# Performance work log

Hardware: AMD Instinct MI355X
Metric: run time of the kernel (lower is better)

The kernel has to match this reference:

```python
import jax, jax.numpy as jnp
import numpy as np

EPS = 1e-5


def conv1x1(x, w, b):
    # x: [b,c,h,w], w: [o,c], b: [o] -> [b,o,h,w]  (1x1 conv == channel matmul)
    return jnp.einsum('bchw,oc->bohw', x, w) + b[None, :, None, None]


def nor_mean_std(x):
    # instance norm over spatial dims (torch calc_mean_std uses unbiased var)
    mean = jnp.mean(x, axis=(2, 3), keepdims=True)
    var = jnp.var(x, axis=(2, 3), keepdims=True, ddof=1)
    return (x - mean) / jnp.sqrt(var + EPS)


def nor_mean(x):
    mean = jnp.mean(x, axis=(2, 3), keepdims=True)
    return x - mean, mean


def net(x, w1, b1, w2, b2):
    return conv1x1(jax.nn.relu(conv1x1(x, w1, b1)), w2, b2)


def setup_inputs() -> dict:
    key = jax.random.key(0)
    ks = jax.random.split(key, 8)
    B, C, H, W = 8, 256, 128, 128
    return {
        'content': jax.random.normal(ks[0], (B, C, H, W), jnp.float32),
        'style': jax.random.normal(ks[1], (B, C, H, W), jnp.float32),
        'w1': jax.random.normal(ks[2], (128, 256), jnp.float32) * 0.05,
        'b1': jax.random.normal(ks[3], (128,), jnp.float32) * 0.05,
        'w2': jax.random.normal(ks[4], (32, 128), jnp.float32) * 0.05,
        'b2': jax.random.normal(ks[5], (32,), jnp.float32) * 0.05,
        'wu': jax.random.normal(ks[6], (256, 32), jnp.float32) * 0.05,
        'bu': jax.random.normal(ks[7], (256,), jnp.float32) * 0.05,
    }


def reference(content, style, w1, b1, w2, b2, wu, bu):
    cF_nor = nor_mean_std(content)
    sF_nor, smean = nor_mean(style)
    cF = net(cF_nor, w1, b1, w2, b2)          # [b,32,h,w]
    sF = net(sF_nor, w1, b1, w2, b2)          # [b,32,h,w]
    b, c, h, w = cF.shape
    hw = h * w
    sf = sF.reshape(b, c, hw)
    # channel covariance: [b,32,32]
    s_cov = jnp.einsum('bcn,bdn->bcd', sf, sf) / hw
    s_cov = jax.nn.softmax(s_cov, axis=-1) * (c ** -0.5)
    gF = jnp.einsum('bcd,bdn->bcn', s_cov, cF.reshape(b, c, hw)).reshape(b, c, h, w)
    gF = conv1x1(gF, wu, bu)                  # [b,256,h,w]
    return gF + smean + content
```

## Files before the change

### kernel.cpp

```cpp
#include <hip/hip_runtime.h>

#define HW 16384
#define C_IN 256
#define C_MID 128
#define C_OUT 32
#define EPSF 1e-5f

typedef __bf16 bf16x8 __attribute__((ext_vector_type(8)));
typedef __bf16 bf16x4 __attribute__((ext_vector_type(4)));
typedef float f32x4 __attribute__((ext_vector_type(4)));

__device__ __forceinline__ bf16x4 cvt4(f32x4 v) {
    bf16x4 r;
    r[0] = (__bf16)v[0]; r[1] = (__bf16)v[1];
    r[2] = (__bf16)v[2]; r[3] = (__bf16)v[3];
    return r;
}

__global__ __launch_bounds__(512) void k_stats10(const float* __restrict__ content,
                                                 const float* __restrict__ style,
                                                 float* __restrict__ cmean,
                                                 float* __restrict__ crstd,
                                                 float* __restrict__ smean,
                                                 __bf16* __restrict__ cbf,
                                                 __bf16* __restrict__ sbf) {
    const int bc = blockIdx.x;
    const int t = threadIdx.x;
    const f32x4* cp = (const f32x4*)(content + (size_t)bc * HW);
    const f32x4* sp = (const f32x4*)(style + (size_t)bc * HW);
    const int phase = (bc * 257) & 4095;

    int idx[8];
    #pragma unroll
    for (int i = 0; i < 8; ++i) idx[i] = (phase + t + i * 512) & 4095;

    f32x4 c[8], s[8];
    #pragma unroll
    for (int i = 0; i < 8; ++i) c[i] = __builtin_nontemporal_load(cp + idx[i]);
    #pragma unroll
    for (int i = 0; i < 8; ++i) s[i] = __builtin_nontemporal_load(sp + idx[i]);
    asm volatile("" ::
        "v"(c[0]), "v"(c[1]), "v"(c[2]), "v"(c[3]), "v"(c[4]), "v"(c[5]), "v"(c[6]), "v"(c[7]),
        "v"(s[0]), "v"(s[1]), "v"(s[2]), "v"(s[3]), "v"(s[4]), "v"(s[5]), "v"(s[6]), "v"(s[7]));

    {
        bf16x4* cb = (bf16x4*)(cbf + (size_t)bc * HW);
        bf16x4* sb = (bf16x4*)(sbf + (size_t)bc * HW);
        #pragma unroll
        for (int i = 0; i < 8; ++i) {
            cb[idx[i]] = cvt4(c[i]);
            sb[idx[i]] = cvt4(s[i]);
        }
    }

    float cs, cq, ss;
    {
        f32x4 a01 = c[0] + c[1], a23 = c[2] + c[3], a45 = c[4] + c[5], a67 = c[6] + c[7];
        f32x4 a = (a01 + a23) + (a45 + a67);
        cs = (a[0] + a[1]) + (a[2] + a[3]);
        f32x4 q01 = c[0]*c[0] + c[1]*c[1], q23 = c[2]*c[2] + c[3]*c[3];
        f32x4 q45 = c[4]*c[4] + c[5]*c[5], q67 = c[6]*c[6] + c[7]*c[7];
        f32x4 q = (q01 + q23) + (q45 + q67);
        cq = (q[0] + q[1]) + (q[2] + q[3]);
        f32x4 b01 = s[0] + s[1], b23 = s[2] + s[3], b45 = s[4] + s[5], b67 = s[6] + s[7];
        f32x4 bsum = (b01 + b23) + (b45 + b67);
        ss = (bsum[0] + bsum[1]) + (bsum[2] + bsum[3]);
    }

    #pragma unroll
    for (int d = 32; d > 0; d >>= 1) {
        cs += __shfl_xor(cs, d, 64);
        cq += __shfl_xor(cq, d, 64);
        ss += __shfl_xor(ss, d, 64);
    }
    __shared__ float rs[8], rq[8], rss[8];
    const int wv = t >> 6;
    if ((t & 63) == 0) { rs[wv] = cs; rq[wv] = cq; rss[wv] = ss; }
    __syncthreads();
    if (t == 0) {
        float S = 0.f, Q = 0.f, SS = 0.f;
        #pragma unroll
        for (int i = 0; i < 8; ++i) { S += rs[i]; Q += rq[i]; SS += rss[i]; }
        float n = (float)HW;
        float var = (Q - S * S / n) / (n - 1.f);
        cmean[bc] = S / n;
        crstd[bc] = 1.f / sqrtf(var + EPSF);
        smean[bc] = SS / n;
    }
}

__global__ __launch_bounds__(256) void k_wprep2(const float* __restrict__ w1,
                                                const float* __restrict__ b1,
                                                const float* __restrict__ w2,
                                                const float* __restrict__ cmean,
                                                const float* __restrict__ crstd,
                                                const float* __restrict__ smean,
                                                __bf16* __restrict__ W1c,
                                                float* __restrict__ bias1c,
                                                __bf16* __restrict__ W1s,
                                                float* __restrict__ bias1s,
                                                __bf16* __restrict__ W2b) {
    int o = blockIdx.x, b = blockIdx.y, t = threadIdx.x;
    float w = w1[o * 256 + t];
    float r = crstd[b * 256 + t];
    float wc = w * r;
    W1c[((size_t)(b * 128 + o)) * 256 + t] = (__bf16)wc;
    if (b == 0) {
        W1s[o * 256 + t] = (__bf16)w;
        if (t < 32) W2b[o * 32 + t] = (__bf16)w2[o * 32 + t];
    }
    float pc = wc * cmean[b * 256 + t];
    float ps = w * smean[b * 256 + t];
    __shared__ float rA[256], rB[256];
    rA[t] = pc; rB[t] = ps;
    __syncthreads();
    for (int off = 128; off > 0; off >>= 1) {
        if (t < off) { rA[t] += rA[t + off]; rB[t] += rB[t + off]; }
        __syncthreads();
    }
    if (t == 0) {
        bias1c[b * 128 + o] = b1[o] - rA[0];
        bias1s[b * 128 + o] = b1[o] - rB[0];
    }
}

__global__ __launch_bounds__(256) void k_net_s(const __bf16* __restrict__ x,
                                               const __bf16* __restrict__ W1,
                                               const float* __restrict__ bias1,
                                               const __bf16* __restrict__ W2,
                                               const float* __restrict__ b2,
                                               float* __restrict__ partial) {
    __shared__ __bf16 Xl[64 * 256];
    __shared__ __bf16 Tl[64 * 128];
    const int tid = threadIdx.x;
    const int l = tid & 63, wv = tid >> 6;
    const int lr = l & 15, g = l >> 4;
    const int sw = (lr & 7) << 4;
    const int p0 = blockIdx.x * 64;
    const int b = blockIdx.y;
    const __bf16* xb = x + (size_t)b * C_IN * HW;

    {
        const int p = wv * 16 + lr;
        const __bf16* xp = xb + p0 + p;
        char* row = (char*)&Xl[p * 256];
        #pragma unroll 4
        for (int cc = 0; cc < 16; ++cc) {
            const int c = cc * 16 + g * 4;
            bf16x4 v;
            v[0] = xp[(size_t)(c + 0) * HW];
            v[1] = xp[(size_t)(c + 1) * HW];
            v[2] = xp[(size_t)(c + 2) * HW];
            v[3] = xp[(size_t)(c + 3) * HW];
            *(bf16x4*)(row + ((c * 2) ^ sw)) = v;
        }
    }
    __syncthreads();

    const f32x4 zero4 = {0.f, 0.f, 0.f, 0.f};
    f32x4 acc[2][4];
    #pragma unroll
    for (int mt = 0; mt < 2; ++mt)
        #pragma unroll
        for (int nt = 0; nt < 4; ++nt) acc[mt][nt] = zero4;

    const __bf16* wrow0 = W1 + (size_t)(wv * 32 + lr) * 256 + g * 8;
    const __bf16* wrow1 = wrow0 + 16 * 256;

    #pragma unroll
    for (int kt = 0; kt < 8; ++kt) {
        bf16x8 a0 = *(const bf16x8*)(wrow0 + kt * 32);
        bf16x8 a1 = *(const bf16x8*)(wrow1 + kt * 32);
        #pragma unroll
        for (int nt = 0; nt < 4; ++nt) {
            const char* xrow = (const char*)&Xl[(nt * 16 + lr) * 256];
            bf16x8 bfr = *(const bf16x8*)(xrow + (((kt * 32 + g * 8) * 2) ^ sw));
            acc[0][nt] = __builtin_amdgcn_mfma_f32_16x16x32_bf16(a0, bfr, acc[0][nt], 0, 0, 0);
            acc[1][nt] = __builtin_amdgcn_mfma_f32_16x16x32_bf16(a1, bfr, acc[1][nt], 0, 0, 0);
        }
    }

    float4 bia[2];
    bia[0] = *(const float4*)&bias1[b * 128 + wv * 32 + g * 4];
    bia[1] = *(const float4*)&bias1[b * 128 + wv * 32 + 16 + g * 4];
    __syncthreads();
    #pragma unroll
    for (int mt = 0; mt < 2; ++mt) {
        #pragma unroll
        for (int nt = 0; nt < 4; ++nt) {
            const int p = nt * 16 + lr;
            char* trow = (char*)&Tl[p * 128];
            const int ob = (wv * 32 + mt * 16 + g * 4) * 2;
            bf16x4 tv;
            tv[0] = (__bf16)fmaxf(acc[mt][nt][0] + bia[mt].x, 0.f);
            tv[1] = (__bf16)fmaxf(acc[mt][nt][1] + bia[mt].y, 0.f);
            tv[2] = (__bf16)fmaxf(acc[mt][nt][2] + bia[mt].z, 0.f);
            tv[3] = (__bf16)fmaxf(acc[mt][nt][3] + bia[mt].w, 0.f);
            *(bf16x4*)(trow + (ob ^ sw)) = tv;
        }
    }
    __syncthreads();

    f32x4 acc2[2];
    acc2[0] = zero4; acc2[1] = zero4;
    const int p = wv * 16 + lr;
    const char* trow = (const char*)&Tl[p * 128];
    const __bf16* w2r0 = W2 + (size_t)lr * 128 + g * 8;
    const __bf16* w2r1 = w2r0 + 16 * 128;
    #pragma unroll
    for (int kt = 0; kt < 4; ++kt) {
        bf16x8 bfr = *(const bf16x8*)(trow + (((kt * 32 + g * 8) * 2) ^ sw));
        bf16x8 a0 = *(const bf16x8*)(w2r0 + kt * 32);
        bf16x8 a1 = *(const bf16x8*)(w2r1 + kt * 32);
        acc2[0] = __builtin_amdgcn_mfma_f32_16x16x32_bf16(a0, bfr, acc2[0], 0, 0, 0);
        acc2[1] = __builtin_amdgcn_mfma_f32_16x16x32_bf16(a1, bfr, acc2[1], 0, 0, 0);
    }
    float4 bb0 = *(const float4*)&b2[g * 4];
    float4 bb1 = *(const float4*)&b2[16 + g * 4];
    const int o0 = g * 4;

    float* gt = (float*)Xl;
    gt[(o0 + 0) * 65 + p] = acc2[0][0] + bb0.x;
    gt[(o0 + 1) * 65 + p] = acc2[0][1] + bb0.y;
    gt[(o0 + 2) * 65 + p] = acc2[0][2] + bb0.z;
    gt[(o0 + 3) * 65 + p] = acc2[0][3] + bb0.w;
    gt[(16 + o0 + 0) * 65 + p] = acc2[1][0] + bb1.x;
    gt[(16 + o0 + 1) * 65 + p] = acc2[1][1] + bb1.y;
    gt[(16 + o0 + 2) * 65 + p] = acc2[1][2] + bb1.z;
    gt[(16 + o0 + 3) * 65 + p] = acc2[1][3] + bb1.w;
    __syncthreads();
    const int gi = tid >> 3, jb = (tid & 7) * 4;
    float g4[4] = {0.f, 0.f, 0.f, 0.f};
    #pragma unroll 8
    for (int n = 0; n < 64; ++n) {
        float si = gt[gi * 65 + n];
        #pragma unroll
        for (int q = 0; q < 4; ++q)
            g4[q] = fmaf(si, gt[(jb + q) * 65 + n], g4[q]);
    }
    float* dst = partial + ((size_t)(b * 256 + blockIdx.x)) * 1024 + tid * 4;
    #pragma unroll
    for (int q = 0; q < 4; ++q) dst[q] = g4[q];
}

__global__ __launch_bounds__(1024) void k_softmax2(const float* __restrict__ partial,
                                                   float* __restrict__ scov) {
    int b = blockIdx.x;
    int j = threadIdx.x, i = threadIdx.y;
    const float* base = partial + (size_t)b * 256 * 1024 + i * 32 + j;
    float v0 = 0.f, v1 = 0.f, v2 = 0.f, v3 = 0.f;
    #pragma unroll 4
    for (int s = 0; s < 256; s += 4) {
        v0 += base[(s + 0) * 1024];
        v1 += base[(s + 1) * 1024];
        v2 += base[(s + 2) * 1024];
        v3 += base[(s + 3) * 1024];
    }
    float v = ((v0 + v1) + (v2 + v3)) * (1.f / (float)HW);
    float m = v;
    #pragma unroll
    for (int d = 16; d > 0; d >>= 1) m = fmaxf(m, __shfl_xor(m, d, 32));
    float e = expf(v - m);
    float sum = e;
    #pragma unroll
    for (int d = 16; d > 0; d >>= 1) sum += __shfl_xor(sum, d, 32);
    scov[(size_t)b * 1024 + i * 32 + j] = e / sum * 0.17677669529663687f;
}

__global__ __launch_bounds__(256) void k_netc_final(const __bf16* __restrict__ x,
                                                    const __bf16* __restrict__ W1,
                                                    const float* __restrict__ bias1,
                                                    const __bf16* __restrict__ W2,
                                                    const float* __restrict__ b2,
                                                    const float* __restrict__ scov,
                                                    const float* __restrict__ wu,
                                                    const float* __restrict__ bu,
                                                    const float* __restrict__ smean,
                                                    float* __restrict__ out) {
    __shared__ __bf16 Xl[64 * 256];
    __shared__ __bf16 Tl[64 * 128];
    __shared__ float sCov[1024];
    __shared__ float sG[32 * 64];
    const int tid = threadIdx.x;
    const int l = tid & 63, wv = tid >> 6;
    const int lr = l & 15, g = l >> 4;
    const int sw = (lr & 7) << 4;
    const int p0 = blockIdx.x * 64;
    const int b = blockIdx.y;
    const __bf16* xb = x + (size_t)b * C_IN * HW;

    #pragma unroll
    for (int q = 0; q < 4; ++q)
        sCov[tid + 256 * q] = scov[(size_t)b * 1024 + tid + 256 * q];
    {
        const int p = wv * 16 + lr;
        const __bf16* xp = xb + p0 + p;
        char* row = (char*)&Xl[p * 256];
        #pragma unroll 4
        for (int cc = 0; cc < 16; ++cc) {
            const int c = cc * 16 + g * 4;
            bf16x4 v;
            v[0] = xp[(size_t)(c + 0) * HW];
            v[1] = xp[(size_t)(c + 1) * HW];
            v[2] = xp[(size_t)(c + 2) * HW];
            v[3] = xp[(size_t)(c + 3) * HW];
            *(bf16x4*)(row + ((c * 2) ^ sw)) = v;
        }
    }
    __syncthreads();

    const f32x4 zero4 = {0.f, 0.f, 0.f, 0.f};
    f32x4 acc1[2][4];
    #pragma unroll
    for (int mt = 0; mt < 2; ++mt)
        #pragma unroll
        for (int nt = 0; nt < 4; ++nt) acc1[mt][nt] = zero4;

    const __bf16* W1b = W1 + ((size_t)b << 15);
    const __bf16* wrow0 = W1b + (size_t)(wv * 32 + lr) * 256 + g * 8;
    const __bf16* wrow1 = wrow0 + 16 * 256;

    #pragma unroll
    for (int kt = 0; kt < 8; ++kt) {
        bf16x8 a0 = *(const bf16x8*)(wrow0 + kt * 32);
        bf16x8 a1 = *(const bf16x8*)(wrow1 + kt * 32);
        #pragma unroll
        for (int nt = 0; nt < 4; ++nt) {
            const char* xrow = (const char*)&Xl[(nt * 16 + lr) * 256];
            bf16x8 bfr = *(const bf16x8*)(xrow + (((kt * 32 + g * 8) * 2) ^ sw));
            acc1[0][nt] = __builtin_amdgcn_mfma_f32_16x16x32_bf16(a0, bfr, acc1[0][nt], 0, 0, 0);
            acc1[1][nt] = __builtin_amdgcn_mfma_f32_16x16x32_bf16(a1, bfr, acc1[1][nt], 0, 0, 0);
        }
    }

    float4 bia[2];
    bia[0] = *(const float4*)&bias1[b * 128 + wv * 32 + g * 4];
    bia[1] = *(const float4*)&bias1[b * 128 + wv * 32 + 16 + g * 4];
    #pragma unroll
    for (int mt = 0; mt < 2; ++mt) {
        #pragma unroll
        for (int nt = 0; nt < 4; ++nt) {
            const int p = nt * 16 + lr;
            char* trow = (char*)&Tl[p * 128];
            const int ob = (wv * 32 + mt * 16 + g * 4) * 2;
            bf16x4 tv;
            tv[0] = (__bf16)fmaxf(acc1[mt][nt][0] + bia[mt].x, 0.f);
            tv[1] = (__bf16)fmaxf(acc1[mt][nt][1] + bia[mt].y, 0.f);
            tv[2] = (__bf16)fmaxf(acc1[mt][nt][2] + bia[mt].z, 0.f);
            tv[3] = (__bf16)fmaxf(acc1[mt][nt][3] + bia[mt].w, 0.f);
            *(bf16x4*)(trow + (ob ^ sw)) = tv;
        }
    }
    __syncthreads();

    f32x4 acc2[2];
    acc2[0] = zero4; acc2[1] = zero4;
    const int p = wv * 16 + lr;
    {
        const char* trow = (const char*)&Tl[p * 128];
        const __bf16* w2r0 = W2 + (size_t)lr * 128 + g * 8;
        const __bf16* w2r1 = w2r0 + 16 * 128;
        #pragma unroll
        for (int kt = 0; kt < 4; ++kt) {
            bf16x8 bfr = *(const bf16x8*)(trow + (((kt * 32 + g * 8) * 2) ^ sw));
            bf16x8 a0 = *(const bf16x8*)(w2r0 + kt * 32);
            bf16x8 a1 = *(const bf16x8*)(w2r1 + kt * 32);
            acc2[0] = __builtin_amdgcn_mfma_f32_16x16x32_bf16(a0, bfr, acc2[0], 0, 0, 0);
            acc2[1] = __builtin_amdgcn_mfma_f32_16x16x32_bf16(a1, bfr, acc2[1], 0, 0, 0);
        }
    }
    float4 bb0 = *(const float4*)&b2[g * 4];
    float4 bb1 = *(const float4*)&b2[16 + g * 4];
    const int o0 = g * 4;

    __syncthreads();
    float* sC = (float*)Tl;
    sC[(o0 + 0) * 64 + p] = acc2[0][0] + bb0.x;
    sC[(o0 + 1) * 64 + p] = acc2[0][1] + bb0.y;
    sC[(o0 + 2) * 64 + p] = acc2[0][2] + bb0.z;
    sC[(o0 + 3) * 64 + p] = acc2[0][3] + bb0.w;
    sC[(16 + o0 + 0) * 64 + p] = acc2[1][0] + bb1.x;
    sC[(16 + o0 + 1) * 64 + p] = acc2[1][1] + bb1.y;
    sC[(16 + o0 + 2) * 64 + p] = acc2[1][2] + bb1.z;
    sC[(16 + o0 + 3) * 64 + p] = acc2[1][3] + bb1.w;
    __syncthreads();

    {
        int gp = tid & 63, gib = (tid >> 6) * 8;
        #pragma unroll
        for (int rr = 0; rr < 8; ++rr) {
            int gi = gib + rr;
            float a = 0.f;
            #pragma unroll
            for (int k = 0; k < 32; ++k)
                a = fmaf(sCov[gi * 32 + k], sC[k * 64 + gp], a);
            sG[gi * 64 + gp] = a;
        }
    }
    __syncthreads();

    const int tx = tid & 7, ty = tid >> 3;
    const float* wurow = wu + (size_t)(ty * 8) * 32;
    float acc[8][8];
    #pragma unroll
    for (int i = 0; i < 8; ++i)
        #pragma unroll
        for (int j = 0; j < 8; ++j) acc[i][j] = 0.f;
    #pragma unroll 4
    for (int k = 0; k < 32; ++k) {
        float a[8];
        #pragma unroll
        for (int i = 0; i < 8; ++i) a[i] = wurow[i * 32 + k];
        float4 b4a = *(const float4*)&sG[k * 64 + tx * 8];
        float4 b4b = *(const float4*)&sG[k * 64 + tx * 8 + 4];
        float bb[8] = {b4a.x, b4a.y, b4a.z, b4a.w, b4b.x, b4b.y, b4b.z, b4b.w};
        #pragma unroll
        for (int i = 0; i < 8; ++i)
            #pragma unroll
            for (int j = 0; j < 8; ++j)
                acc[i][j] = fmaf(a[i], bb[j], acc[i][j]);
    }
    float cvv[8][8];
    #pragma unroll
    for (int j = 0; j < 8; ++j) {
        const int pl = tx * 8 + j;
        bf16x8 rv = *(const bf16x8*)((const char*)Xl + pl * 512 + ((ty * 16) ^ (j << 4)));
        #pragma unroll
        for (int i = 0; i < 8; ++i) cvv[i][j] = (float)rv[i];
    }
    #pragma unroll
    for (int i = 0; i < 8; ++i) {
        int o = ty * 8 + i;
        float add = bu[o] + smean[b * 256 + o];
        float* dst = out + (size_t)b * C_IN * HW + (size_t)o * HW + p0 + tx * 8;
        f32x4 r0 = {acc[i][0] + add + cvv[i][0], acc[i][1] + add + cvv[i][1],
                    acc[i][2] + add + cvv[i][2], acc[i][3] + add + cvv[i][3]};
        f32x4 r1 = {acc[i][4] + add + cvv[i][4], acc[i][5] + add + cvv[i][5],
                    acc[i][6] + add + cvv[i][6], acc[i][7] + add + cvv[i][7]};
        __builtin_nontemporal_store(r0, (f32x4*)dst);
        __builtin_nontemporal_store(r1, (f32x4*)(dst + 4));
    }
}

extern "C" void kernel_launch(void* const* d_in, const int* in_sizes, int n_in,
                              void* d_out, int out_size, void* d_ws, size_t ws_size,
                              hipStream_t stream) {
    const float* content = (const float*)d_in[0];
    const float* style   = (const float*)d_in[1];
    const float* w1      = (const float*)d_in[2];
    const float* b1      = (const float*)d_in[3];
    const float* w2      = (const float*)d_in[4];
    const float* b2      = (const float*)d_in[5];
    const float* wu      = (const float*)d_in[6];
    const float* bu      = (const float*)d_in[7];
    float* out = (float*)d_out;
    float* ws  = (float*)d_ws;

    float* cmean   = ws;
    float* crstd   = ws + 2048;
    float* smean   = ws + 4096;
    float* scov    = ws + 6144;
    float* bias1c  = ws + 14336;
    float* bias1s  = ws + 15360;
    __bf16* W2b    = (__bf16*)(ws + 16384);
    __bf16* W1s    = (__bf16*)(ws + 18432);
    __bf16* W1c    = (__bf16*)(ws + 34816);
    float* partial = ws + 165888;
    __bf16* cbf    = (__bf16*)(ws + 2263040);
    __bf16* sbf    = (__bf16*)(ws + 19040256);

    k_stats10<<<dim3(2048), 512, 0, stream>>>(content, style, cmean, crstd, smean, cbf, sbf);
    k_wprep2<<<dim3(128, 8), 256, 0, stream>>>(w1, b1, w2, cmean, crstd, smean,
                                               W1c, bias1c, W1s, bias1s, W2b);
    k_net_s<<<dim3(256, 8), 256, 0, stream>>>(sbf, W1s, bias1s, W2b, b2, partial);
    k_softmax2<<<dim3(8), dim3(32, 32), 0, stream>>>(partial, scov);
    k_netc_final<<<dim3(256, 8), 256, 0, stream>>>(cbf, W1c, bias1c, W2b, b2,
                                                   scov, wu, bu, smean, out);
}
```

Baseline: 223.0 us.

## Split stats and weight-prep into style and content passes reordered for cache reuse

Splits the combined statistics kernel and the weight-prep kernel into separate style and content versions. The content versions are scheduled after the style network and softmax, right before the final content kernel. The aim is for content data and its bf16 copy to still be resident in last-level cache when the final kernel reads them. It adds two extra kernel launches and smaller per-kernel memory parallelism.

Result: no change. 224.2 us (+0.6%).

```diff
diff --git a/kernel.cpp b/kernel.cpp
--- a/kernel.cpp
+++ b/kernel.cpp
@@ -17,16 +17,11 @@
     return r;
 }
 
-__global__ __launch_bounds__(512) void k_stats10(const float* __restrict__ content,
-                                                 const float* __restrict__ style,
-                                                 float* __restrict__ cmean,
-                                                 float* __restrict__ crstd,
+__global__ __launch_bounds__(512) void k_stats_s(const float* __restrict__ style,
                                                  float* __restrict__ smean,
-                                                 __bf16* __restrict__ cbf,
                                                  __bf16* __restrict__ sbf) {
     const int bc = blockIdx.x;
     const int t = threadIdx.x;
-    const f32x4* cp = (const f32x4*)(content + (size_t)bc * HW);
     const f32x4* sp = (const f32x4*)(style + (size_t)bc * HW);
     const int phase = (bc * 257) & 4095;
 
@@ -34,94 +29,135 @@
     #pragma unroll
     for (int i = 0; i < 8; ++i) idx[i] = (phase + t + i * 512) & 4095;
 
-    f32x4 c[8], s[8];
-    #pragma unroll
-    for (int i = 0; i < 8; ++i) c[i] = __builtin_nontemporal_load(cp + idx[i]);
+    f32x4 s[8];
     #pragma unroll
     for (int i = 0; i < 8; ++i) s[i] = __builtin_nontemporal_load(sp + idx[i]);
     asm volatile("" ::
-        "v"(c[0]), "v"(c[1]), "v"(c[2]), "v"(c[3]), "v"(c[4]), "v"(c[5]), "v"(c[6]), "v"(c[7]),
-        "v"(s[0]), "v"(s[1]), "v"(s[2]), "v"(s[3]), "v"(s[4]), "v"(s[5]), "v"(s[6]), "v"(s[7]));
+        "v"(s[0]), "v"(s[1]), "v"(s[2]), "v"(s[3]),
+        "v"(s[4]), "v"(s[5]), "v"(s[6]), "v"(s[7]));
+
+    {
+        bf16x4* sb = (bf16x4*)(sbf + (size_t)bc * HW);
+        #pragma unroll
+        for (int i = 0; i < 8; ++i) sb[idx[i]] = cvt4(s[i]);
+    }
+
+    f32x4 a01 = s[0] + s[1], a23 = s[2] + s[3], a45 = s[4] + s[5], a67 = s[6] + s[7];
+    f32x4 a = (a01 + a23) + (a45 + a67);
+    float ss = (a[0] + a[1]) + (a[2] + a[3]);
+
+    #pragma unroll
+    for (int d = 32; d > 0; d >>= 1) ss += __shfl_xor(ss, d, 64);
+    __shared__ float rss[8];
+    const int wv = t >> 6;
+    if ((t & 63) == 0) rss[wv] = ss;
+    __syncthreads();
+    if (t == 0) {
+        float S = 0.f;
+        #pragma unroll
+        for (int i = 0; i < 8; ++i) S += rss[i];
+        smean[bc] = S / (float)HW;
+    }
+}
+
+__global__ __launch_bounds__(512) void k_stats_c(const float* __restrict__ content,
+                                                 float* __restrict__ cmean,
+                                                 float* __restrict__ crstd,
+                                                 __bf16* __restrict__ cbf) {
+    const int bc = blockIdx.x;
+    const int t = threadIdx.x;
+    const f32x4* cp = (const f32x4*)(content + (size_t)bc * HW);
+    const int phase = (bc * 257) & 4095;
+
+    int idx[8];
+    #pragma unroll
+    for (int i = 0; i < 8; ++i) idx[i] = (phase + t + i * 512) & 4095;
+
+    f32x4 c[8];
+    #pragma unroll
+    for (int i = 0; i < 8; ++i) c[i] = __builtin_nontemporal_load(cp + idx[i]);
+    asm volatile("" ::
+        "v"(c[0]), "v"(c[1]), "v"(c[2]), "v"(c[3]),
+        "v"(c[4]), "v"(c[5]), "v"(c[6]), "v"(c[7]));
 
     {
         bf16x4* cb = (bf16x4*)(cbf + (size_t)bc * HW);
-        bf16x4* sb = (bf16x4*)(sbf + (size_t)bc * HW);
-        #pragma unroll
-        for (int i = 0; i < 8; ++i) {
-            cb[idx[i]] = cvt4(c[i]);
-            sb[idx[i]] = cvt4(s[i]);
-        }
-    }
-
-    float cs, cq, ss;
-    {
-        f32x4 a01 = c[0] + c[1], a23 = c[2] + c[3], a45 = c[4] + c[5], a67 = c[6] + c[7];
-        f32x4 a = (a01 + a23) + (a45 + a67);
-        cs = (a[0] + a[1]) + (a[2] + a[3]);
-        f32x4 q01 = c[0]*c[0] + c[1]*c[1], q23 = c[2]*c[2] + c[3]*c[3];
-        f32x4 q45 = c[4]*c[4] + c[5]*c[5], q67 = c[6]*c[6] + c[7]*c[7];
-        f32x4 q = (q01 + q23) + (q45 + q67);
-        cq = (q[0] + q[1]) + (q[2] + q[3]);
-        f32x4 b01 = s[0] + s[1], b23 = s[2] + s[3], b45 = s[4] + s[5], b67 = s[6] + s[7];
-        f32x4 bsum = (b01 + b23) + (b45 + b67);
-        ss = (bsum[0] + bsum[1]) + (bsum[2] + bsum[3]);
-    }
+        #pragma unroll
+        for (int i = 0; i < 8; ++i) cb[idx[i]] = cvt4(c[i]);
+    }
+
+    f32x4 a01 = c[0] + c[1], a23 = c[2] + c[3], a45 = c[4] + c[5], a67 = c[6] + c[7];
+    f32x4 a = (a01 + a23) + (a45 + a67);
+    float cs = (a[0] + a[1]) + (a[2] + a[3]);
+    f32x4 q01 = c[0]*c[0] + c[1]*c[1], q23 = c[2]*c[2] + c[3]*c[3];
+    f32x4 q45 = c[4]*c[4] + c[5]*c[5], q67 = c[6]*c[6] + c[7]*c[7];
+    f32x4 q = (q01 + q23) + (q45 + q67);
+    float cq = (q[0] + q[1]) + (q[2] + q[3]);
 
     #pragma unroll
     for (int d = 32; d > 0; d >>= 1) {
         cs += __shfl_xor(cs, d, 64);
         cq += __shfl_xor(cq, d, 64);
-        ss += __shfl_xor(ss, d, 64);
-    }
-    __shared__ float rs[8], rq[8], rss[8];
+    }
+    __shared__ float rs[8], rq[8];
     const int wv = t >> 6;
-    if ((t & 63) == 0) { rs[wv] = cs; rq[wv] = cq; rss[wv] = ss; }
+    if ((t & 63) == 0) { rs[wv] = cs; rq[wv] = cq; }
     __syncthreads();
     if (t == 0) {
-        float S = 0.f, Q = 0.f, SS = 0.f;
-        #pragma unroll
-        for (int i = 0; i < 8; ++i) { S += rs[i]; Q += rq[i]; SS += rss[i]; }
+        float S = 0.f, Q = 0.f;
+        #pragma unroll
+        for (int i = 0; i < 8; ++i) { S += rs[i]; Q += rq[i]; }
         float n = (float)HW;
         float var = (Q - S * S / n) / (n - 1.f);
         cmean[bc] = S / n;
         crstd[bc] = 1.f / sqrtf(var + EPSF);
-        smean[bc] = SS / n;
-    }
-}
-
-__global__ __launch_bounds__(256) void k_wprep2(const float* __restrict__ w1,
-                                                const float* __restrict__ b1,
-                                                const float* __restrict__ w2,
-                                                const float* __restrict__ cmean,
-                                                const float* __restrict__ crstd,
-                                                const float* __restrict__ smean,
-                                                __bf16* __restrict__ W1c,
-                                                float* __restrict__ bias1c,
-                                                __bf16* __restrict__ W1s,
-                                                float* __restrict__ bias1s,
-                                                __bf16* __restrict__ W2b) {
+    }
+}
+
+__global__ __launch_bounds__(256) void k_wprep_s(const float* __restrict__ w1,
+                                                 const float* __restrict__ b1,
+                                                 const float* __restrict__ w2,
+                                                 const float* __restrict__ smean,
+                                                 __bf16* __restrict__ W1s,
+                                                 float* __restrict__ bias1s,
+                                                 __bf16* __restrict__ W2b) {
+    int o = blockIdx.x, b = blockIdx.y, t = threadIdx.x;
+    float w = w1[o * 256 + t];
+    if (b == 0) {
+        W1s[o * 256 + t] = (__bf16)w;
+        if (t < 32) W2b[o * 32 + t] = (__bf16)w2[o * 32 + t];
+    }
+    float ps = w * smean[b * 256 + t];
+    __shared__ float rB[256];
+    rB[t] = ps;
+    __syncthreads();
+    for (int off = 128; off > 0; off >>= 1) {
+        if (t < off) rB[t] += rB[t + off];
+        __syncthreads();
+    }
+    if (t == 0) bias1s[b * 128 + o] = b1[o] - rB[0];
+}
+
+__global__ __launch_bounds__(256) void k_wprep_c(const float* __restrict__ w1,
+                                                 const float* __restrict__ b1,
+                                                 const float* __restrict__ cmean,
+                                                 const float* __restrict__ crstd,
+                                                 __bf16* __restrict__ W1c,
+                                                 float* __restrict__ bias1c) {
     int o = blockIdx.x, b = blockIdx.y, t = threadIdx.x;
     float w = w1[o * 256 + t];
     float r = crstd[b * 256 + t];
     float wc = w * r;
     W1c[((size_t)(b * 128 + o)) * 256 + t] = (__bf16)wc;
-    if (b == 0) {
-        W1s[o * 256 + t] = (__bf16)w;
-        if (t < 32) W2b[o * 32 + t] = (__bf16)w2[o * 32 + t];
-    }
     float pc = wc * cmean[b * 256 + t];
-    float ps = w * smean[b * 256 + t];
-    __shared__ float rA[256], rB[256];
-    rA[t] = pc; rB[t] = ps;
+    __shared__ float rA[256];
+    rA[t] = pc;
     __syncthreads();
     for (int off = 128; off > 0; off >>= 1) {
-        if (t < off) { rA[t] += rA[t + off]; rB[t] += rB[t + off]; }
+        if (t < off) rA[t] += rA[t + off];
         __syncthreads();
     }
-    if (t == 0) {
-        bias1c[b * 128 + o] = b1[o] - rA[0];
-        bias1s[b * 128 + o] = b1[o] - rB[0];
-    }
+    if (t == 0) bias1c[b * 128 + o] = b1[o] - rA[0];
 }
 
 __global__ __launch_bounds__(256) void k_net_s(const __bf16* __restrict__ x,
@@ -469,11 +505,12 @@
     __bf16* cbf    = (__bf16*)(ws + 2263040);
     __bf16* sbf    = (__bf16*)(ws + 19040256);
 
-    k_stats10<<<dim3(2048), 512, 0, stream>>>(content, style, cmean, crstd, smean, cbf, sbf);
-    k_wprep2<<<dim3(128, 8), 256, 0, stream>>>(w1, b1, w2, cmean, crstd, smean,
-                                               W1c, bias1c, W1s, bias1s, W2b);
+    k_stats_s<<<dim3(2048), 512, 0, stream>>>(style, smean, sbf);
+    k_wprep_s<<<dim3(128, 8), 256, 0, stream>>>(w1, b1, w2, smean, W1s, bias1s, W2b);
     k_net_s<<<dim3(256, 8), 256, 0, stream>>>(sbf, W1s, bias1s, W2b, b2, partial);
     k_softmax2<<<dim3(8), dim3(32, 32), 0, stream>>>(partial, scov);
+    k_stats_c<<<dim3(2048), 512, 0, stream>>>(content, cmean, crstd, cbf);
+    k_wprep_c<<<dim3(128, 8), 256, 0, stream>>>(w1, b1, cmean, crstd, W1c, bias1c);
     k_netc_final<<<dim3(256, 8), 256, 0, stream>>>(cbf, W1c, bias1c, W2b, b2,
                                                    scov, wu, bu, smean, out);
 }
```
